# Optimization experiments

Measured on AMD Instinct MI355X. Metric: run time of the kernel, lower is better.

Reference implementation:

```python
import jax, jax.numpy as jnp
import numpy as np

VOCAB, EMB, ATT = 100000, 128, 128
N_CODES, N_ANC = 100000, 8

def setup_inputs() -> dict:
    key = jax.random.key(0)
    k1, k2, k3, k4, k5 = jax.random.split(key, 5)
    return {
        "W_emb": jax.random.normal(k1, (VOCAB, EMB), dtype=jnp.float32),
        "W_attention": jax.random.normal(k2, (2 * EMB, ATT), dtype=jnp.float32) * 0.05,
        "b_attention": jnp.zeros((ATT,), dtype=jnp.float32),
        "v_attention": jax.random.normal(k3, (ATT,), dtype=jnp.float32) * 0.05,
        "leaves": jax.random.randint(k4, (N_CODES, N_ANC), 0, VOCAB, dtype=jnp.int64),
        "ancestors": jax.random.randint(k5, (N_CODES, N_ANC), 0, VOCAB, dtype=jnp.int64),
    }

def reference(W_emb, W_attention, b_attention, v_attention, leaves, ancestors):
    # gather: [N, A, E] each
    leave_emb = W_emb[leaves]
    anc_emb = W_emb[ancestors]
    attention_input = jnp.concatenate((leave_emb, anc_emb), axis=2)  # [N, A, 2E]
    mlp = jnp.tanh(jnp.einsum('nae,ed->nad', attention_input, W_attention) + b_attention)
    pre_attention = jnp.einsum('nad,d->na', mlp, v_attention)  # [N, A]
    attn = jax.nn.softmax(pre_attention, axis=1)
    # attention-weighted sum over ancestors: [N, E]
    return jnp.einsum('nae,na->ne', anc_emb, attn)
```

## Files before the change

kernel.cpp:

```cpp
#include <hip/hip_runtime.h>
#include <hip/hip_bf16.h>
#include <hip/hip_fp8.h>

#define VOCAB  100000
#define EMB    128
#define NCODES 100000
#define NANC   8

#define ATT_GRID 1250
#define ATT_TPB  5
#define PRE_GRID 1250
#define PRE_TPB  5

typedef __attribute__((ext_vector_type(8))) short    short8;
typedef __attribute__((ext_vector_type(4))) float    float4v;
typedef __attribute__((ext_vector_type(2))) float    floatx2;
typedef __attribute__((ext_vector_type(4))) unsigned uint4v;
typedef __attribute__((ext_vector_type(2))) __bf16   bf16x2;

__device__ __forceinline__ ushort f2bf(float x) {
    unsigned u = __float_as_uint(x);
    u += 0x7fffu + ((u >> 16) & 1u);
    return (ushort)(u >> 16);
}
__device__ __forceinline__ float bf2f(ushort h) {
    return __uint_as_float((unsigned)h << 16);
}
__device__ __forceinline__ unsigned pk2bf(float lo, float hi) {
    bf16x2 v;
    v[0] = (__bf16)lo;
    v[1] = (__bf16)hi;
    return __builtin_bit_cast(unsigned, v);
}
__device__ __forceinline__ unsigned char f2fp8(float x) {
    __hip_fp8_e4m3 t(x);
    return t.__x;
}
__device__ __forceinline__ unsigned pack_fp8x4(float a, float b, float c, float d) {
#if __has_builtin(__builtin_amdgcn_cvt_pk_fp8_f32)
    int w = __builtin_amdgcn_cvt_pk_fp8_f32(a, b, 0, false);
    w = __builtin_amdgcn_cvt_pk_fp8_f32(c, d, w, true);
    return (unsigned)w;
#else
    return (unsigned)f2fp8(a) | ((unsigned)f2fp8(b) << 8)
         | ((unsigned)f2fp8(c) << 16) | ((unsigned)f2fp8(d) << 24);
#endif
}
template <bool HI>
__device__ __forceinline__ floatx2 fp8pair(unsigned v) {
#if __has_builtin(__builtin_amdgcn_cvt_pk_f32_fp8)
    return __builtin_amdgcn_cvt_pk_f32_fp8((int)v, HI);
#else
    __hip_fp8_e4m3 a, b;
    const unsigned s = HI ? 16u : 0u;
    a.__x = (v >> s) & 0xffu;
    b.__x = (v >> (s + 8u)) & 0xffu;
    floatx2 r; r[0] = (float)a; r[1] = (float)b; return r;
#endif
}

__device__ __forceinline__ void tanh2pk(floatx2 za, floatx2 zb,
                                        floatx2& ta, floatx2& tb) {
    floatx2 xa, xb;
    xa[0] = fminf(fmaxf(za[0], -3.5f), 3.5f);
    xa[1] = fminf(fmaxf(za[1], -3.5f), 3.5f);
    xb[0] = fminf(fmaxf(zb[0], -3.5f), 3.5f);
    xb[1] = fminf(fmaxf(zb[1], -3.5f), 3.5f);
    const floatx2 ya = xa * xa, yb = xb * xb;
    floatx2 Na = ya + 105.0f;  Na = ya * Na + 945.0f;
    floatx2 Nb = yb + 105.0f;  Nb = yb * Nb + 945.0f;
    floatx2 Da = ya * 15.0f + 420.0f;  Da = ya * Da + 945.0f;
    floatx2 Db = yb * 15.0f + 420.0f;  Db = yb * Db + 945.0f;
    const floatx2 Dp = Da * Db;
    const float r = __builtin_amdgcn_rcpf(Dp[0] * Dp[1]);
    floatx2 qv;  qv[0] = r * Dp[1];  qv[1] = r * Dp[0];
    const floatx2 ia = qv * Db;
    const floatx2 ib = qv * Da;
    ta = (xa * Na) * ia;
    tb = (xb * Nb) * ib;
}

__global__ void transpose_watt(const float* __restrict__ W_att,
                               ushort* __restrict__ WT)
{
    const int id = blockIdx.x * 256 + threadIdx.x;
    const int c = id >> 7, e = id & 127;
    const int h = c >> 7, d = c & 127;
    WT[c * 128 + e] = f2bf(W_att[(h * 128 + e) * 128 + d]);
}

__global__ __launch_bounds__(256) void precompute(
    const float*  __restrict__ W_emb,
    const ushort* __restrict__ WT,
    const float*  __restrict__ b_att,
    unsigned char* __restrict__ P1,
    unsigned char* __restrict__ M)
{
    const int t = threadIdx.x, wave = t >> 6, lane = t & 63;
    const int n15 = lane & 15, quad = lane >> 4;
    const int cw = wave * 64;

    short8 wfrag[4][4];
    #pragma unroll
    for (int ntl = 0; ntl < 4; ++ntl) {
        const int c = cw + ((n15 >> 2) << 4) + ntl * 4 + (n15 & 3);
        #pragma unroll
        for (int kt = 0; kt < 4; ++kt)
            wfrag[kt][ntl] = *(const short8*)(WT + c * 128 + kt * 32 + quad * 8);
    }

    float4 bb[4];
    #pragma unroll
    for (int ntl = 0; ntl < 4; ++ntl) {
        if (wave < 2) bb[ntl] = *(const float4*)(b_att + cw + quad * 16 + ntl * 4);
        else          bb[ntl] = make_float4(0.f, 0.f, 0.f, 0.f);
    }

    unsigned char* Pt;
    size_t rstride;
    int cbase;
    if (wave < 2) { Pt = P1; rstride = 128; cbase = cw + quad * 16; }
    else          { Pt = M;  rstride = 384; cbase = (cw - 128) + quad * 16; }

    const int b = blockIdx.x;

#define LOAD_TILE(dst, rtv)                                                   \
    {                                                                         \
        const float4v* src =                                                  \
            (const float4v*)(W_emb + (size_t)((rtv) * 16 + n15) * 128);       \
        _Pragma("unroll")                                                     \
        for (int kt = 0; kt < 4; ++kt) {                                      \
            (dst)[2 * kt]     = __builtin_nontemporal_load(src + kt * 8 + quad * 2);     \
            (dst)[2 * kt + 1] = __builtin_nontemporal_load(src + kt * 8 + quad * 2 + 1); \
        }                                                                     \
    }

    float4v buf[3][8];
    LOAD_TILE(buf[0], b)
    LOAD_TILE(buf[1], b + PRE_GRID)

    #pragma unroll
    for (int it = 0; it < PRE_TPB; ++it) {
        if (it + 2 < PRE_TPB)
            LOAD_TILE(buf[(it + 2) % 3], b + (it + 2) * PRE_GRID)

        const float4v* cur = buf[it % 3];
        const int R = (b + it * PRE_GRID) * 16;

        float4v acc[4];
        #pragma unroll
        for (int i = 0; i < 4; ++i) acc[i] = (float4v)0.0f;

        #pragma unroll
        for (int kt = 0; kt < 4; ++kt) {
            const float4v a0 = cur[2 * kt], a1 = cur[2 * kt + 1];
            uint4v ad;
            ad[0] = pk2bf(a0[0], a0[1]);
            ad[1] = pk2bf(a0[2], a0[3]);
            ad[2] = pk2bf(a1[0], a1[1]);
            ad[3] = pk2bf(a1[2], a1[3]);
            const short8 af = __builtin_bit_cast(short8, ad);
            if ((wave < 2) && ((kt >> 1) == wave))
                *(short8*)(M + (size_t)(R + n15) * 384 + 128 + kt * 64 + quad * 16) = af;
            #pragma unroll
            for (int ntl = 0; ntl < 4; ++ntl)
                acc[ntl] = __builtin_amdgcn_mfma_f32_16x16x32_bf16(
                               wfrag[kt][ntl], af, acc[ntl], 0, 0, 0);
        }

        uint4v pks;
        #pragma unroll
        for (int ntl = 0; ntl < 4; ++ntl)
            pks[ntl] = pack_fp8x4(acc[ntl][0] + bb[ntl].x,
                                  acc[ntl][1] + bb[ntl].y,
                                  acc[ntl][2] + bb[ntl].z,
                                  acc[ntl][3] + bb[ntl].w);
        *(uint4v*)(Pt + (size_t)(R + n15) * rstride + cbase) = pks;
    }
#undef LOAD_TILE
}

__global__ __launch_bounds__(256) void attention_main(
    const unsigned char* __restrict__ P1,
    const unsigned char* __restrict__ M,
    const float* __restrict__ v_att,
    const int*   __restrict__ leaves, const int* __restrict__ anc,
    float*       __restrict__ out)
{
    const int t = threadIdx.x;
    const int wave = t >> 6, lane = t & 63;
    const int sub = lane >> 4, l16 = lane & 15;
    const int jj = l16 & 7;

    floatx2 vv[4];
    #pragma unroll
    for (int p = 0; p < 4; ++p)
        vv[p] = *(const floatx2*)(v_att + l16 * 8 + 2 * p);

    const int base = blockIdx.x;

    auto idx_ptr = [&](int tile) -> const int* {
        const int n = tile * 16 + wave * 4 + sub;
        return (l16 & 8) ? (anc + n * 8 + jj) : (leaves + n * 8 + jj);
    };

    int    lf[2][NANC], an[2][NANC];
    uint2  R1[2][NANC], R2[2][NANC];
    short8 EM[NANC];
    int    raw[2];

    raw[0] = __builtin_nontemporal_load(idx_ptr(base));
    #pragma unroll
    for (int a = 0; a < NANC; ++a) {
        lf[0][a] = __shfl(raw[0], (sub << 4) + a);
        an[0][a] = __shfl(raw[0], (sub << 4) + 8 + a);
    }
    #pragma unroll
    for (int a = 0; a < NANC; ++a)
        R1[0][a] = *(const uint2*)(P1 + (size_t)lf[0][a] * 128 + l16 * 8);
    #pragma unroll
    for (int a = 0; a < NANC; ++a)
        R2[0][a] = *(const uint2*)(M + (size_t)an[0][a] * 384 + l16 * 8);
    #pragma unroll
    for (int a = 0; a < NANC; ++a)
        EM[a] = *(const short8*)(M + (size_t)an[0][a] * 384 + 128 + l16 * 16);
    raw[1] = __builtin_nontemporal_load(idx_ptr(base + ATT_GRID));

    #pragma unroll
    for (int it = 0; it < ATT_TPB; ++it) {
        const int cur = it & 1, nx = cur ^ 1;
        const int tile = base + it * ATT_GRID;

        if (it + 1 < ATT_TPB) {
            #pragma unroll
            for (int a = 0; a < NANC; ++a) {
                lf[nx][a] = __shfl(raw[nx], (sub << 4) + a);
                an[nx][a] = __shfl(raw[nx], (sub << 4) + 8 + a);
            }
            #pragma unroll
            for (int a = 0; a < NANC; ++a)
                R1[nx][a] = *(const uint2*)(P1 + (size_t)lf[nx][a] * 128 + l16 * 8);
            #pragma unroll
            for (int a = 0; a < NANC; ++a)
                R2[nx][a] = *(const uint2*)(M + (size_t)an[nx][a] * 384 + l16 * 8);
        }
        if (it + 2 < ATT_TPB)
            raw[cur] = __builtin_nontemporal_load(idx_ptr(tile + 2 * ATT_GRID));

        const int n = tile * 16 + wave * 4 + sub;

        float q[NANC];
        #pragma unroll
        for (int a = 0; a < NANC; ++a) {
            const floatx2 z0 = fp8pair<false>(R1[cur][a].x) + fp8pair<false>(R2[cur][a].x);
            const floatx2 z1 = fp8pair<true >(R1[cur][a].x) + fp8pair<true >(R2[cur][a].x);
            const floatx2 z2 = fp8pair<false>(R1[cur][a].y) + fp8pair<false>(R2[cur][a].y);
            const floatx2 z3 = fp8pair<true >(R1[cur][a].y) + fp8pair<true >(R2[cur][a].y);
            floatx2 t0, t1, t2, t3;
            tanh2pk(z0, z1, t0, t1);
            tanh2pk(z2, z3, t2, t3);
            floatx2 qa = t0 * vv[0];
            qa = t1 * vv[1] + qa;
            qa = t2 * vv[2] + qa;
            qa = t3 * vv[3] + qa;
            q[a] = qa[0] + qa[1];
        }

        float r4[4];
        #pragma unroll
        for (int i = 0; i < 4; ++i) {
            const float keep = (l16 & 8) ? q[i + 4] : q[i];
            const float send = (l16 & 8) ? q[i]     : q[i + 4];
            r4[i] = keep + __shfl_xor(send, 8);
        }
        float s2[2];
        #pragma unroll
        for (int i = 0; i < 2; ++i) {
            const float keep = (l16 & 4) ? r4[i + 2] : r4[i];
            const float send = (l16 & 4) ? r4[i]     : r4[i + 2];
            s2[i] = keep + __shfl_xor(send, 4);
        }
        {
            const float keep = (l16 & 2) ? s2[1] : s2[0];
            const float send = (l16 & 2) ? s2[0] : s2[1];
            s2[0] = keep + __shfl_xor(send, 2);
        }
        float tq = s2[0] + __shfl_xor(s2[0], 1);

        float m = tq;
        m = fmaxf(m, __shfl_xor(m, 8));
        m = fmaxf(m, __shfl_xor(m, 4));
        m = fmaxf(m, __shfl_xor(m, 2));
        const float e = __expf(tq - m);
        float s = e;
        s += __shfl_xor(s, 8); s += __shfl_xor(s, 4); s += __shfl_xor(s, 2);
        const float wl = e * __fdividef(1.0f, s);

        float wa[NANC];
        {
            const float p  = __shfl_xor(wl, 2);
            const float w0 = (l16 & 2) ? p  : wl;
            const float w1 = (l16 & 2) ? wl : p;
            const float p0 = __shfl_xor(w0, 4), p1 = __shfl_xor(w1, 4);
            const float v00 = (l16 & 4) ? p0 : w0, v01 = (l16 & 4) ? p1 : w1;
            const float v10 = (l16 & 4) ? w0 : p0, v11 = (l16 & 4) ? w1 : p1;
            float g;
            g = __shfl_xor(v00, 8); wa[0] = (l16 & 8) ? g : v00; wa[4] = (l16 & 8) ? v00 : g;
            g = __shfl_xor(v01, 8); wa[1] = (l16 & 8) ? g : v01; wa[5] = (l16 & 8) ? v01 : g;
            g = __shfl_xor(v10, 8); wa[2] = (l16 & 8) ? g : v10; wa[6] = (l16 & 8) ? v10 : g;
            g = __shfl_xor(v11, 8); wa[3] = (l16 & 8) ? g : v11; wa[7] = (l16 & 8) ? v11 : g;
        }

        floatx2 o[4] = {(floatx2)0.f, (floatx2)0.f, (floatx2)0.f, (floatx2)0.f};
        #pragma unroll
        for (int a = 0; a < NANC; ++a) {
            floatx2 wv; wv[0] = wa[a]; wv[1] = wa[a];
            #pragma unroll
            for (int p = 0; p < 4; ++p) {
                floatx2 ev;
                ev[0] = bf2f((ushort)EM[a][2 * p]);
                ev[1] = bf2f((ushort)EM[a][2 * p + 1]);
                o[p] = ev * wv + o[p];
            }
        }
        float4v o1, o2;
        o1[0] = o[0][0]; o1[1] = o[0][1]; o1[2] = o[1][0]; o1[3] = o[1][1];
        o2[0] = o[2][0]; o2[1] = o[2][1]; o2[2] = o[3][0]; o2[3] = o[3][1];
        __builtin_nontemporal_store(o1, (float4v*)(out + (size_t)n * 128 + l16 * 8));
        __builtin_nontemporal_store(o2, (float4v*)(out + (size_t)n * 128 + l16 * 8 + 4));

        if (it + 1 < ATT_TPB) {
            #pragma unroll
            for (int a = 0; a < NANC; ++a)
                EM[a] = *(const short8*)(M + (size_t)an[nx][a] * 384 + 128 + l16 * 16);
        }
    }
}

extern "C" void kernel_launch(void* const* d_in, const int* in_sizes, int n_in,
                              void* d_out, int out_size, void* d_ws, size_t ws_size,
                              hipStream_t stream) {
    const float* W_emb  = (const float*)d_in[0];
    const float* W_att  = (const float*)d_in[1];
    const float* b_att  = (const float*)d_in[2];
    const float* v_att  = (const float*)d_in[3];
    const int*   leaves = (const int*)d_in[4];
    const int*   anc    = (const int*)d_in[5];
    float*       out    = (float*)d_out;

    unsigned char* P1 = (unsigned char*)d_ws;
    unsigned char* M  = P1 + (size_t)VOCAB * 128;
    ushort* WT = (ushort*)(M + (size_t)VOCAB * 384);

    transpose_watt<<<128, 256, 0, stream>>>(W_att, WT);
    precompute<<<PRE_GRID, 256, 0, stream>>>(W_emb, WT, b_att, P1, M);
    attention_main<<<ATT_GRID, 256, 0, stream>>>(P1, M, v_att,
                                                 leaves, anc, out);
}
```

Before: 210.4 us.

## Stage W_emb tiles through double-buffered LDS via global_load_lds in precompute

In the precompute kernel, each of the four waves previously loaded the same 16x128 W_emb tile into its own registers, so every tile was fetched from global memory four times. The block now loads each tile once, using the gfx950 global-to-LDS DMA builtin, into a double-buffered shared-memory tile. Waves then read their MFMA operands from LDS, with a barrier each iteration. This removes the redundant global traffic and frees registers, but the prefetch distance drops from two tiles to one and a block-wide sync plus LDS reads are added.

```diff
diff --git a/kernel.cpp b/kernel.cpp
--- a/kernel.cpp
+++ b/kernel.cpp
@@ -96,6 +96,8 @@
     unsigned char* __restrict__ P1,
     unsigned char* __restrict__ M)
 {
+    __shared__ __align__(16) float lds[2 * 2048];
+
     const int t = threadIdx.x, wave = t >> 6, lane = t & 63;
     const int n15 = lane & 15, quad = lane >> 4;
     const int cw = wave * 64;
@@ -124,28 +126,43 @@
 
     const int b = blockIdx.x;
 
-#define LOAD_TILE(dst, rtv)                                                   \
+    const int r0 = t >> 5, cf = (t & 31) * 4;
+
+#if __has_builtin(__builtin_amdgcn_global_load_lds)
+#define DMA_TILE(bufi, rtv)                                                   \
     {                                                                         \
-        const float4v* src =                                                  \
-            (const float4v*)(W_emb + (size_t)((rtv) * 16 + n15) * 128);       \
-        _Pragma("unroll")                                                     \
-        for (int kt = 0; kt < 4; ++kt) {                                      \
-            (dst)[2 * kt]     = __builtin_nontemporal_load(src + kt * 8 + quad * 2);     \
-            (dst)[2 * kt + 1] = __builtin_nontemporal_load(src + kt * 8 + quad * 2 + 1); \
-        }                                                                     \
-    }
-
-    float4v buf[3][8];
-    LOAD_TILE(buf[0], b)
-    LOAD_TILE(buf[1], b + PRE_GRID)
+        const float* tb0 = W_emb + (size_t)(rtv) * 2048;                      \
+        __builtin_amdgcn_global_load_lds(                                     \
+            (const __attribute__((address_space(1))) void*)(tb0 + r0 * 128 + cf), \
+            (__attribute__((address_space(3))) void*)&lds[(bufi) * 2048 + wave * 256], \
+            16, 0, 0);                                                        \
+        __builtin_amdgcn_global_load_lds(                                     \
+            (const __attribute__((address_space(1))) void*)(tb0 + (r0 + 8) * 128 + cf), \
+            (__attribute__((address_space(3))) void*)&lds[(bufi) * 2048 + 1024 + wave * 256], \
+            16, 0, 0);                                                        \
+    }
+#else
+#define DMA_TILE(bufi, rtv)                                                   \
+    {                                                                         \
+        const float* tb0 = W_emb + (size_t)(rtv) * 2048;                      \
+        const float4v v0 = *(const float4v*)(tb0 + r0 * 128 + cf);            \
+        const float4v v1 = *(const float4v*)(tb0 + (r0 + 8) * 128 + cf);      \
+        *(float4v*)&lds[(bufi) * 2048 + t * 4]        = v0;                   \
+        *(float4v*)&lds[(bufi) * 2048 + 1024 + t * 4] = v1;                   \
+    }
+#endif
+
+    DMA_TILE(0, b)
 
     #pragma unroll
     for (int it = 0; it < PRE_TPB; ++it) {
-        if (it + 2 < PRE_TPB)
-            LOAD_TILE(buf[(it + 2) % 3], b + (it + 2) * PRE_GRID)
-
-        const float4v* cur = buf[it % 3];
-        const int R = (b + it * PRE_GRID) * 16;
+        __syncthreads();
+        if (it + 1 < PRE_TPB)
+            DMA_TILE((it + 1) & 1, b + (it + 1) * PRE_GRID)
+
+        const int rt = b + it * PRE_GRID;
+        const int R = rt * 16;
+        const float* lb = &lds[(it & 1) * 2048];
 
         float4v acc[4];
         #pragma unroll
@@ -153,7 +170,8 @@
 
         #pragma unroll
         for (int kt = 0; kt < 4; ++kt) {
-            const float4v a0 = cur[2 * kt], a1 = cur[2 * kt + 1];
+            const float4v a0 = *(const float4v*)&lb[n15 * 128 + kt * 32 + quad * 8];
+            const float4v a1 = *(const float4v*)&lb[n15 * 128 + kt * 32 + quad * 8 + 4];
             uint4v ad;
             ad[0] = pk2bf(a0[0], a0[1]);
             ad[1] = pk2bf(a0[2], a0[3]);
@@ -177,7 +195,7 @@
                                   acc[ntl][3] + bb[ntl].w);
         *(uint4v*)(Pt + (size_t)(R + n15) * rstride + cbase) = pks;
     }
-#undef LOAD_TILE
+#undef DMA_TILE
 }
 
 __global__ __launch_bounds__(256) void attention_main(
```

Measured after the change: 188.9 us. 1.11x faster.
